# Kernel optimization log

Hardware: AMD Instinct MI355X
Metric: run time of the kernel (lower is better)

Reference implementation:

```python
import jax, jax.numpy as jnp
import numpy as np

NUM_CLASSES = 10
LAMBDA_COORD = 5.0
LAMBDA_NOOBJ = 0.5
B, S, P = 2048, 26, 5 + NUM_CLASSES


def setup_inputs() -> dict:
    key = jax.random.key(0)
    k1, k2 = jax.random.split(key)
    predictions = jax.random.normal(k1, (B, S, S, P), dtype=jnp.float32)
    targets = jax.random.normal(k2, (B, S * S * P,), dtype=jnp.float32)
    return {"predictions": predictions, "targets": targets}


def reference(predictions, targets):
    b, s, _, p = predictions.shape
    pred = predictions.reshape(b, s * s, p)          # (B, S*S, 5+C)
    tgt = targets.reshape(b, s * s, -1)              # (B, S*S, 5+C)

    obj = tgt[..., 4] > 0                            # object mask per cell

    # Coordinate loss: lambda_coord * sum((pred_xywh - tgt_xywh)^2) over object cells
    coord_sq = jnp.sum((pred[..., :4] - tgt[..., :4]) ** 2, axis=-1)
    coord_loss = LAMBDA_COORD * jnp.sum(jnp.where(obj, coord_sq, 0.0))

    # Confidence loss: (sigmoid(p_conf) - t_conf)^2 on obj cells,
    # lambda_noobj * sigmoid(p_conf)^2 on no-obj cells (scalar MSE mean == squared diff)
    conf_p = jax.nn.sigmoid(pred[..., 4])
    conf_loss = jnp.sum(jnp.where(obj,
                                  (conf_p - tgt[..., 4]) ** 2,
                                  LAMBDA_NOOBJ * conf_p ** 2))

    # Classification loss: mean over C of squared diff per object cell, summed
    cls_sq = jnp.mean((pred[..., 5:5 + NUM_CLASSES] - tgt[..., 5:5 + NUM_CLASSES]) ** 2, axis=-1)
    class_loss = jnp.sum(jnp.where(obj, cls_sq, 0.0))

    total_loss = coord_loss + conf_loss + class_loss
    return (total_loss, coord_loss, conf_loss, class_loss)
```

## Files before the change

### kernel.cpp

```cpp
#include <hip/hip_runtime.h>

typedef float f4v __attribute__((ext_vector_type(4)));

constexpr int   NUM_CLASSES  = 10;
constexpr float LAMBDA_COORD = 5.0f;
constexpr float LAMBDA_NOOBJ = 0.5f;
constexpr int   BLOCK = 256;
constexpr int   NBLOCKS_MAX = 2028;
constexpr int   LDST_W = 288;

#define GLOAD_LDS16(gp, lp) \
    __builtin_amdgcn_global_load_lds( \
        (const __attribute__((address_space(1))) void*)(gp), \
        (__attribute__((address_space(3))) void*)(lp), 16, 0, 0)
#define WAITVM(n)  asm volatile("s_waitcnt vmcnt(" #n ")" ::: "memory")
#define WAITLGKM() asm volatile("s_waitcnt lgkmcnt(0)" ::: "memory")
#define SB()       __builtin_amdgcn_sched_barrier(0)

__device__ __forceinline__ void slot(const f4v p, const f4v t,
                                     const float t4a, const float t4b,
                                     unsigned j0,
                                     float& coord, float& conf, float& cls)
{
#pragma unroll
    for (int m = 0; m < 4; ++m) {
        unsigned j  = j0 + (unsigned)m;
        float d     = p[m] - t[m];
        float sq    = d * d;
        float t4    = (j >= 15u) ? t4b : t4a;
        float sqo   = (t4 > 0.f) ? sq : 0.f;
        coord += ((j - 4u) >= 11u) ? sqo : 0.f;
        cls   += ((j - 5u) <  10u) ? sqo : 0.f;
    }
    bool  hasConf = (j0 - 1u) < 4u;
    float pc = (j0 == 4u) ? p[0]
             : (j0 == 3u) ? p[1]
             : (j0 == 2u) ? p[2]
             :              p[3];
    float e   = __expf(-pc);
    float sig = 1.f / (1.f + e);
    bool  obj = t4a > 0.f;
    float dsv = sig - t4a;
    float confv = obj ? dsv * dsv : LAMBDA_NOOBJ * sig * sig;
    conf += hasConf ? confv : 0.f;
}

#define STAGE(LBUF, TT, PREG, HREG) do {                                     \
    unsigned kk_ = idx + (unsigned)(TT) * S;                                 \
    PREG = __builtin_nontemporal_load((const f4v*)pred4 + kk_);              \
    GLOAD_LDS16((const f4v*)tgt4 + kk_, (LBUF) + 12 + 4 * lane);             \
    if (lane < 7u) {                                                         \
        int kw_ = (int)(kk_ - lane);                                         \
        int hs_ = (lane < 3u) ? kw_ - 3 + (int)lane : kw_ + 61 + (int)lane;  \
        hs_ = hs_ < 0 ? 0 : hs_;                                             \
        hs_ = hs_ > (int)n4 - 1 ? (int)n4 - 1 : hs_;                         \
        HREG = *((const f4v*)tgt4 + hs_);                                    \
    }                                                                        \
} while (0)

#define CLOAD(LBUF, TT, HREG, TV, AV, BV, JV) do {                           \
    if (lane < 7u) {                                                         \
        int off_ = (lane < 3u) ? 4 * (int)lane : 268 + 4 * ((int)lane - 3);  \
        *(f4v*)((LBUF) + off_) = HREG;                                       \
    }                                                                        \
    unsigned kk_ = idx + (unsigned)(TT) * S;                                 \
    JV = (4u * kk_) % 15u;                                                   \
    int q_ = 4 * (int)lane + 16 - (int)JV;                                   \
    TV = *(const f4v*)((LBUF) + 12 + 4 * lane);                              \
    AV = (LBUF)[q_];                                                         \
    BV = (LBUF)[q_ + ((JV >= 12u) ? 15 : 0)];                                \
} while (0)

__global__ __launch_bounds__(BLOCK) void yolo_main(
    const float* __restrict__ pred4,
    const float* __restrict__ tgt4,
    float* __restrict__ ws,
    unsigned n4, unsigned nblocks)
{
    __shared__ float ldsT[4][2][LDST_W];

    const unsigned tid  = threadIdx.x;
    const unsigned lane = tid & 63u;
    const unsigned wv   = tid >> 6;
    const unsigned S    = nblocks * 256u;
    const unsigned idx  = blockIdx.x * 256u + tid;
    const unsigned NTu  = n4 / S;

    float* L0 = &ldsT[wv][0][0];
    float* L1 = &ldsT[wv][1][0];

    float coord = 0.f, conf = 0.f, cls = 0.f;
    f4v pA = {0,0,0,0}, pB = {0,0,0,0}, hA = {0,0,0,0}, hB = {0,0,0,0};

    if (NTu >= 2u) {
        STAGE(L0, 0, pA, hA); SB();
        STAGE(L1, 1, pB, hB); SB();
        unsigned T = 0;
        for (; T + 1u < NTu; T += 2u) {
            WAITVM(3); SB();
            f4v tA; float aA, bA; unsigned jA;
            CLOAD(L0, T, hA, tA, aA, bA, jA);
            WAITLGKM(); SB();
            f4v puA = pA;
            if (T + 2u < NTu) { STAGE(L0, T + 2u, pA, hA); }
            SB();
            slot(puA, tA, aA, bA, jA, coord, conf, cls);

            if (T + 2u < NTu) { WAITVM(3); } else { WAITVM(0); }
            SB();
            f4v tB; float aB, bB; unsigned jB;
            CLOAD(L1, T + 1u, hB, tB, aB, bB, jB);
            WAITLGKM(); SB();
            f4v puB = pB;
            if (T + 3u < NTu) { STAGE(L1, T + 3u, pB, hB); }
            SB();
            slot(puB, tB, aB, bB, jB, coord, conf, cls);
        }
        if (T < NTu) {
            WAITVM(0); SB();
            f4v tA; float aA, bA; unsigned jA;
            CLOAD(L0, T, hA, tA, aA, bA, jA);
            WAITLGKM(); SB();
            slot(pA, tA, aA, bA, jA, coord, conf, cls);
        }
    } else if (NTu == 1u) {
        STAGE(L0, 0, pA, hA); SB();
        WAITVM(0); SB();
        f4v tA; float aA, bA; unsigned jA;
        CLOAD(L0, 0, hA, tA, aA, bA, jA);
        WAITLGKM(); SB();
        slot(pA, tA, aA, bA, jA, coord, conf, cls);
    }

    for (unsigned k = NTu * S + idx; k < n4; k += S) {
        f4v p = *((const f4v*)pred4 + k);
        f4v t = *((const f4v*)tgt4 + k);
        unsigned base  = 4u * k;
        unsigned cell0 = base / 15u;
        unsigned c15   = cell0 * 15u;
        unsigned j0    = base - c15;
        float ta = tgt4[c15 + 4u];
        float tb = tgt4[(j0 >= 12u) ? c15 + 19u : c15 + 4u];
        slot(p, t, ta, tb, j0, coord, conf, cls);
    }

#pragma unroll
    for (int off = 32; off > 0; off >>= 1) {
        coord += __shfl_down(coord, off);
        conf  += __shfl_down(conf,  off);
        cls   += __shfl_down(cls,   off);
    }

    __shared__ float s[3][4];
    if (lane == 0) { s[0][wv] = coord; s[1][wv] = conf; s[2][wv] = cls; }
    __syncthreads();

    if (tid == 0) {
        float c0 = s[0][0] + s[0][1] + s[0][2] + s[0][3];
        float c1 = s[1][0] + s[1][1] + s[1][2] + s[1][3];
        float c2 = s[2][0] + s[2][1] + s[2][2] + s[2][3];
        ws[blockIdx.x]               = c0;
        ws[nblocks + blockIdx.x]     = c1;
        ws[2 * nblocks + blockIdx.x] = c2;
    }
}

__global__ __launch_bounds__(BLOCK) void yolo_finalize(
    const float* __restrict__ ws, float* __restrict__ out, unsigned nblocks)
{
    float c0 = 0.f, c1 = 0.f, c2 = 0.f;
    for (unsigned i = threadIdx.x; i < nblocks; i += BLOCK) {
        c0 += ws[i];
        c1 += ws[nblocks + i];
        c2 += ws[2 * nblocks + i];
    }
#pragma unroll
    for (int off = 32; off > 0; off >>= 1) {
        c0 += __shfl_down(c0, off);
        c1 += __shfl_down(c1, off);
        c2 += __shfl_down(c2, off);
    }
    __shared__ float s[3][4];
    int wave = threadIdx.x >> 6, lane = threadIdx.x & 63;
    if (lane == 0) { s[0][wave] = c0; s[1][wave] = c1; s[2][wave] = c2; }
    __syncthreads();
    if (threadIdx.x == 0) {
        float coord = LAMBDA_COORD * (s[0][0] + s[0][1] + s[0][2] + s[0][3]);
        float conf  =                 s[1][0] + s[1][1] + s[1][2] + s[1][3];
        float cls   = (1.f / NUM_CLASSES) * (s[2][0] + s[2][1] + s[2][2] + s[2][3]);
        out[0] = coord + conf + cls;
        out[1] = coord;
        out[2] = conf;
        out[3] = cls;
    }
}

extern "C" void kernel_launch(void* const* d_in, const int* in_sizes, int n_in,
                              void* d_out, int out_size, void* d_ws, size_t ws_size,
                              hipStream_t stream) {
    const float* pred = (const float*)d_in[0];
    const float* tgt  = (const float*)d_in[1];
    float* out = (float*)d_out;
    float* ws  = (float*)d_ws;

    unsigned total = (unsigned)in_sizes[0];
    unsigned n4    = total / 4u;

    unsigned nblocks = NBLOCKS_MAX;
    size_t need = (size_t)nblocks * 3 * sizeof(float);
    if (need > ws_size) nblocks = (unsigned)(ws_size / (3 * sizeof(float)));

    yolo_main<<<nblocks, BLOCK, 0, stream>>>(pred, tgt, ws, n4, nblocks);
    yolo_finalize<<<1, BLOCK, 0, stream>>>(ws, out, nblocks);
}
```

Before: 179.5 us.

## Replace LDS-staged target tiles with register loads and tiny per-wave conf LDS

Target float4s now go straight into registers instead of through global_load_lds into a per-wave LDS tile with halo loads. Each lane writes only the confidence value of any cell it holds into a small per-wave LDS array. One extra scalar global load per lane fetches the boundary cell's confidence, and each lane then reads its cell's objectness from that array. This cuts LDS traffic and footprint, and drops the seven-lane halo loads, at the cost of more index arithmetic and an LDS write-then-read round trip in every iteration.

Measured after the change: 179.6 us. No clear change (+0.0%).

```diff
diff --git a/kernel.cpp b/kernel.cpp
--- a/kernel.cpp
+++ b/kernel.cpp
@@ -7,13 +7,10 @@
 constexpr float LAMBDA_NOOBJ = 0.5f;
 constexpr int   BLOCK = 256;
 constexpr int   NBLOCKS_MAX = 2028;
-constexpr int   LDST_W = 288;
-
-#define GLOAD_LDS16(gp, lp) \
-    __builtin_amdgcn_global_load_lds( \
-        (const __attribute__((address_space(1))) void*)(gp), \
-        (__attribute__((address_space(3))) void*)(lp), 16, 0, 0)
-#define WAITVM(n)  asm volatile("s_waitcnt vmcnt(" #n ")" ::: "memory")
+constexpr int   LCONF = 20;
+
+#define WAITVM3()  asm volatile("s_waitcnt vmcnt(3)" ::: "memory")
+#define WAITVM0()  asm volatile("s_waitcnt vmcnt(0)" ::: "memory")
 #define WAITLGKM() asm volatile("s_waitcnt lgkmcnt(0)" ::: "memory")
 #define SB()       __builtin_amdgcn_sched_barrier(0)
 
@@ -45,39 +42,47 @@
     conf += hasConf ? confv : 0.f;
 }
 
-#define STAGE(LBUF, TT, PREG, HREG) do {                                     \
-    unsigned kk_ = idx + (unsigned)(TT) * S;                                 \
-    PREG = __builtin_nontemporal_load((const f4v*)pred4 + kk_);              \
-    GLOAD_LDS16((const f4v*)tgt4 + kk_, (LBUF) + 12 + 4 * lane);             \
-    if (lane < 7u) {                                                         \
-        int kw_ = (int)(kk_ - lane);                                         \
-        int hs_ = (lane < 3u) ? kw_ - 3 + (int)lane : kw_ + 61 + (int)lane;  \
-        hs_ = hs_ < 0 ? 0 : hs_;                                             \
-        hs_ = hs_ > (int)n4 - 1 ? (int)n4 - 1 : hs_;                         \
-        HREG = *((const f4v*)tgt4 + hs_);                                    \
-    }                                                                        \
+#define STAGE(TT, PREG, TREG, BREG) do {                                   \
+    unsigned kk_ = idx + (unsigned)(TT) * S;                               \
+    PREG = __builtin_nontemporal_load((const f4v*)pred + kk_);             \
+    TREG = *((const f4v*)tgtp + kk_);                                      \
+    unsigned wb_  = 4u * (kk_ - lane);             \
+    unsigned cl_  = wb_ / 15u;                                             \
+    unsigned wo_  = wb_ - cl_ * 15u;                   \
+    unsigned rB_  = (wo_ >= 5u) ? 0u : 17u;      \
+    unsigned pos_ = wb_ - wo_ + rB_ * 15u + 4u;                            \
+    if (pos_ >= fTot) pos_ = fTot - 1u;          \
+    BREG = tgtp[pos_];                           \
 } while (0)
 
-#define CLOAD(LBUF, TT, HREG, TV, AV, BV, JV) do {                           \
-    if (lane < 7u) {                                                         \
-        int off_ = (lane < 3u) ? 4 * (int)lane : 268 + 4 * ((int)lane - 3);  \
-        *(f4v*)((LBUF) + off_) = HREG;                                       \
-    }                                                                        \
-    unsigned kk_ = idx + (unsigned)(TT) * S;                                 \
-    JV = (4u * kk_) % 15u;                                                   \
-    int q_ = 4 * (int)lane + 16 - (int)JV;                                   \
-    TV = *(const f4v*)((LBUF) + 12 + 4 * lane);                              \
-    AV = (LBUF)[q_];                                                         \
-    BV = (LBUF)[q_ + ((JV >= 12u) ? 15 : 0)];                                \
+#define CONSUME(TT, PREG, TREG, BREG) do {                                 \
+    unsigned kk_ = idx + (unsigned)(TT) * S;                               \
+    unsigned wb_ = 4u * (kk_ - lane);                                      \
+    unsigned cl_ = wb_ / 15u;                                              \
+    unsigned wo_ = wb_ - cl_ * 15u;                                        \
+    unsigned rB_ = (wo_ >= 5u) ? 0u : 17u;                                 \
+    unsigned x_  = wo_ + 4u * lane;                            \
+    unsigned q_  = (x_ * 2185u) >> 15;           \
+    unsigned j0_ = x_ - q_ * 15u;                      \
+    if (lane == 0u) Lc[wv][rB_] = BREG;                                    \
+    if (j0_ - 1u < 4u) {                        \
+        float cv_ = (j0_ == 4u) ? TREG[0] : (j0_ == 3u) ? TREG[1]          \
+                  : (j0_ == 2u) ? TREG[2] : TREG[3];                       \
+        Lc[wv][q_] = cv_;                                                  \
+    }                                                                      \
+    WAITLGKM(); SB();                             \
+    float a_ = Lc[wv][q_];                                                 \
+    float b_ = Lc[wv][q_ + ((j0_ >= 12u) ? 1u : 0u)];                      \
+    slot(PREG, TREG, a_, b_, j0_, coord, conf, cls);                       \
 } while (0)
 
 __global__ __launch_bounds__(BLOCK) void yolo_main(
-    const float* __restrict__ pred4,
-    const float* __restrict__ tgt4,
+    const float* __restrict__ pred,
+    const float* __restrict__ tgtp,
     float* __restrict__ ws,
     unsigned n4, unsigned nblocks)
 {
-    __shared__ float ldsT[4][2][LDST_W];
+    __shared__ float Lc[4][LCONF];
 
     const unsigned tid  = threadIdx.x;
     const unsigned lane = tid & 63u;
@@ -85,62 +90,49 @@
     const unsigned S    = nblocks * 256u;
     const unsigned idx  = blockIdx.x * 256u + tid;
     const unsigned NTu  = n4 / S;
-
-    float* L0 = &ldsT[wv][0][0];
-    float* L1 = &ldsT[wv][1][0];
+    const unsigned fTot = 4u * n4;
 
     float coord = 0.f, conf = 0.f, cls = 0.f;
-    f4v pA = {0,0,0,0}, pB = {0,0,0,0}, hA = {0,0,0,0}, hB = {0,0,0,0};
+    f4v pA = {0,0,0,0}, tA = {0,0,0,0}, pB = {0,0,0,0}, tB = {0,0,0,0};
+    float bA = 0.f, bB = 0.f;
 
     if (NTu >= 2u) {
-        STAGE(L0, 0, pA, hA); SB();
-        STAGE(L1, 1, pB, hB); SB();
+        STAGE(0, pA, tA, bA); SB();
+        STAGE(1, pB, tB, bB); SB();
         unsigned T = 0;
         for (; T + 1u < NTu; T += 2u) {
-            WAITVM(3); SB();
-            f4v tA; float aA, bA; unsigned jA;
-            CLOAD(L0, T, hA, tA, aA, bA, jA);
-            WAITLGKM(); SB();
-            f4v puA = pA;
-            if (T + 2u < NTu) { STAGE(L0, T + 2u, pA, hA); }
+            WAITVM3(); SB();
+            f4v pu = pA, tu = tA; float bu = bA;
+            if (T + 2u < NTu) { STAGE(T + 2u, pA, tA, bA); }
             SB();
-            slot(puA, tA, aA, bA, jA, coord, conf, cls);
-
-            if (T + 2u < NTu) { WAITVM(3); } else { WAITVM(0); }
+            CONSUME(T, pu, tu, bu);
+
+            if (T + 3u < NTu) { WAITVM3(); } else { WAITVM0(); }
             SB();
-            f4v tB; float aB, bB; unsigned jB;
-            CLOAD(L1, T + 1u, hB, tB, aB, bB, jB);
-            WAITLGKM(); SB();
-            f4v puB = pB;
-            if (T + 3u < NTu) { STAGE(L1, T + 3u, pB, hB); }
+            f4v pv = pB, tv = tB; float bv = bB;
+            if (T + 3u < NTu) { STAGE(T + 3u, pB, tB, bB); }
             SB();
-            slot(puB, tB, aB, bB, jB, coord, conf, cls);
+            CONSUME(T + 1u, pv, tv, bv);
         }
         if (T < NTu) {
-            WAITVM(0); SB();
-            f4v tA; float aA, bA; unsigned jA;
-            CLOAD(L0, T, hA, tA, aA, bA, jA);
-            WAITLGKM(); SB();
-            slot(pA, tA, aA, bA, jA, coord, conf, cls);
+            WAITVM0(); SB();
+            CONSUME(T, pA, tA, bA);
         }
     } else if (NTu == 1u) {
-        STAGE(L0, 0, pA, hA); SB();
-        WAITVM(0); SB();
-        f4v tA; float aA, bA; unsigned jA;
-        CLOAD(L0, 0, hA, tA, aA, bA, jA);
-        WAITLGKM(); SB();
-        slot(pA, tA, aA, bA, jA, coord, conf, cls);
+        STAGE(0, pA, tA, bA); SB();
+        WAITVM0(); SB();
+        CONSUME(0, pA, tA, bA);
     }
 
     for (unsigned k = NTu * S + idx; k < n4; k += S) {
-        f4v p = *((const f4v*)pred4 + k);
-        f4v t = *((const f4v*)tgt4 + k);
+        f4v p = *((const f4v*)pred + k);
+        f4v t = *((const f4v*)tgtp + k);
         unsigned base  = 4u * k;
         unsigned cell0 = base / 15u;
         unsigned c15   = cell0 * 15u;
         unsigned j0    = base - c15;
-        float ta = tgt4[c15 + 4u];
-        float tb = tgt4[(j0 >= 12u) ? c15 + 19u : c15 + 4u];
+        float ta = tgtp[c15 + 4u];
+        float tb = tgtp[(j0 >= 12u) ? c15 + 19u : c15 + 4u];
         slot(p, t, ta, tb, j0, coord, conf, cls);
     }
 
```
